# Optimization experiments

Hardware: AMD Instinct MI355X
Metric: run time of the kernel (lower is better)

The kernel has to match this reference:

```python
import jax, jax.numpy as jnp
import numpy as np

BLOCK = 64
# NF4 codebook (normal-float 4-bit values, as in QLoRA/torchao)
NF4_TABLE = jnp.array([
    -1.0, -0.6961928009986877, -0.5250730514526367, -0.39491748809814453,
    -0.28444138169288635, -0.18477343022823334, -0.09105003625154495, 0.0,
    0.07958029955625534, 0.16093020141124725, 0.24611230194568634,
    0.33791524171829224, 0.44070982933044434, 0.5626170039176941,
    0.7229568362236023, 1.0], dtype=jnp.float32)

D_MODEL, HIDDEN = 4096, 11008
BATCH, SEQ = 2, 2048


def setup_inputs() -> dict:
    key = jax.random.key(0)
    ks = jax.random.split(key, 7)
    x = jax.random.normal(ks[0], (BATCH, SEQ, D_MODEL), dtype=jnp.float32)
    w1_q = jax.random.randint(ks[1], (HIDDEN, D_MODEL), 0, 16, dtype=jnp.int32)
    w2_q = jax.random.randint(ks[2], (HIDDEN, D_MODEL), 0, 16, dtype=jnp.int32)
    w3_q = jax.random.randint(ks[3], (D_MODEL, HIDDEN), 0, 16, dtype=jnp.int32)
    # per-block absmax scales (positive, typical weight magnitude ~0.02)
    w1_scale = jax.random.uniform(ks[4], (HIDDEN, D_MODEL // BLOCK), dtype=jnp.float32) * 0.04
    w2_scale = jax.random.uniform(ks[5], (HIDDEN, D_MODEL // BLOCK), dtype=jnp.float32) * 0.04
    w3_scale = jax.random.uniform(ks[6], (D_MODEL, HIDDEN // BLOCK), dtype=jnp.float32) * 0.04
    return {"x": x, "w1_q": w1_q, "w1_scale": w1_scale,
            "w2_q": w2_q, "w2_scale": w2_scale,
            "w3_q": w3_q, "w3_scale": w3_scale}


def dequant_nf4(q, scale):
    # q: [O, I] int codes in [0,16); scale: [O, I//BLOCK]
    O, I = q.shape
    vals = NF4_TABLE[q]                               # lookup -> [O, I]
    vals = vals.reshape(O, I // BLOCK, BLOCK) * scale[:, :, None]
    return vals.reshape(O, I)


def reference(x, w1_q, w1_scale, w2_q, w2_scale, w3_q, w3_scale):
    w1 = dequant_nf4(w1_q, w1_scale)                  # [H, D]
    w2 = dequant_nf4(w2_q, w2_scale)                  # [H, D]
    w3 = dequant_nf4(w3_q, w3_scale)                  # [D, H]
    h = jax.nn.silu(jnp.einsum('bsd,hd->bsh', x, w1)) * jnp.einsum('bsd,hd->bsh', x, w2)
    return jnp.einsum('bsh,dh->bsd', h, w3)
```

## Files before the change

### kernel.cpp

```cpp
#include <hip/hip_runtime.h>
#include <hip/hip_bf16.h>

typedef unsigned short u16;
typedef __bf16  bf16x8 __attribute__((ext_vector_type(8)));
typedef float   f32x4  __attribute__((ext_vector_type(4)));

__device__ __constant__ float NF4C[16] = {
    -1.0f, -0.6961928009986877f, -0.5250730514526367f, -0.39491748809814453f,
    -0.28444138169288635f, -0.18477343022823334f, -0.09105003625154495f, 0.0f,
    0.07958029955625534f, 0.16093020141124725f, 0.24611230194568634f,
    0.33791524171829224f, 0.44070982933044434f, 0.5626170039176941f,
    0.7229568362236023f, 1.0f };

__device__ __forceinline__ u16 f2bf(float f) {
    union { float f; unsigned u; } v; v.f = f;
    unsigned r = v.u + 0x7FFFu + ((v.u >> 16) & 1u);
    return (u16)(r >> 16);
}
__device__ __forceinline__ float bf2f(u16 b) {
    union { unsigned u; float f; } v; v.u = ((unsigned)b) << 16;
    return v.f;
}

__device__ __forceinline__ void gl2lds16(const void* g, void* l) {
    __builtin_amdgcn_global_load_lds(
        (__attribute__((address_space(1))) void*)g,
        (__attribute__((address_space(3))) void*)l,
        16, 0, 0);
}

#define WAITVM(N) asm volatile("s_waitcnt vmcnt(" #N ")" ::: "memory")

__global__ __launch_bounds__(256) void cast_f32_bf16(
    const float* __restrict__ in, u16* __restrict__ out, int n8) {
    int i = blockIdx.x * 256 + threadIdx.x;
    if (i >= n8) return;
    const float4* p = (const float4*)in + (size_t)i * 2;
    float4 a = p[0], b = p[1];
    union { u16 u[8]; uint4 v; } r;
    r.u[0] = f2bf(a.x); r.u[1] = f2bf(a.y); r.u[2] = f2bf(a.z); r.u[3] = f2bf(a.w);
    r.u[4] = f2bf(b.x); r.u[5] = f2bf(b.y); r.u[6] = f2bf(b.z); r.u[7] = f2bf(b.w);
    ((uint4*)out)[i] = r.v;
}

__global__ __launch_bounds__(256) void dequant_nf4(
    const int* __restrict__ q, const float* __restrict__ s,
    u16* __restrict__ w, int I, int spr) {
    __shared__ float tab[16];
    if (threadIdx.x < 16) tab[threadIdx.x] = NF4C[threadIdx.x];
    __syncthreads();
    int col = (blockIdx.x * 256 + threadIdx.x) * 8;
    if (col >= I) return;
    int row = blockIdx.y;
    size_t base = (size_t)row * I + col;
    int4 c0 = *(const int4*)(q + base);
    int4 c1 = *(const int4*)(q + base + 4);
    float sc = s[(size_t)row * spr + (col >> 6)];
    union { u16 u[8]; uint4 v; } r;
    r.u[0] = f2bf(tab[c0.x & 15] * sc);
    r.u[1] = f2bf(tab[c0.y & 15] * sc);
    r.u[2] = f2bf(tab[c0.z & 15] * sc);
    r.u[3] = f2bf(tab[c0.w & 15] * sc);
    r.u[4] = f2bf(tab[c1.x & 15] * sc);
    r.u[5] = f2bf(tab[c1.y & 15] * sc);
    r.u[6] = f2bf(tab[c1.z & 15] * sc);
    r.u[7] = f2bf(tab[c1.w & 15] * sc);
    *(uint4*)(w + base) = r.v;
}

template<int EPI>
__global__ __launch_bounds__(512, 2) void gemm_bt(
    const u16* __restrict__ A, const u16* __restrict__ B,
    void* Cout, const u16* gate, int K, int ldc) {
    __shared__ u16 lA[4 * 8192];
    __shared__ u16 lB[4 * 8192];

    const int tid  = threadIdx.x;
    const int lane = tid & 63;
    const int wv   = tid >> 6;

    const int NT = gridDim.x, MT = gridDim.y;
    int id  = blockIdx.y * NT + blockIdx.x;
    int nid = (id & 7) * ((NT * MT) >> 3) + (id >> 3);
    const int bx = nid / MT;
    const int by = nid - bx * MT;

    const int sr = lane >> 2;
    const int sq = (lane & 3) ^ ((sr >> 1) & 3);
    const u16* gA = A + (size_t)(by * 256 + wv * 16 + sr) * K + (sq << 3);
    const u16* gB = B + (size_t)(bx * 256 + wv * 16 + sr) * K + (sq << 3);
    const size_t half = (size_t)128 * K;
    const int stoff = wv * 512 + lane * 8;

    const int r16    = lane & 15;
    const int pq     = lane >> 4;
    const int slot16 = (r16 << 2) + (pq ^ ((r16 >> 1) & 3));
    const int aFrag  = ((wv & 1) << 3) * 512 + slot16 * 8;
    const int bFrag  = ((wv >> 1) << 2) * 512 + slot16 * 8;

#define STAGE(T) do {                                                   \
        const u16* a_ = gA + (size_t)(T) * 32;                          \
        const u16* b_ = gB + (size_t)(T) * 32;                          \
        u16* la_ = lA + (((T) & 3) << 13) + stoff;                      \
        u16* lb_ = lB + (((T) & 3) << 13) + stoff;                      \
        gl2lds16(a_, la_);                                              \
        gl2lds16(a_ + half, la_ + 8 * 512);                             \
        gl2lds16(b_, lb_);                                              \
        gl2lds16(b_ + half, lb_ + 8 * 512);                             \
    } while (0)

#define COMPUTE(T) do {                                                 \
        const u16* sa_ = lA + (((T) & 3) << 13) + aFrag;                \
        const u16* sb_ = lB + (((T) & 3) << 13) + bFrag;                \
        bf16x8 af[8], bfr[4];                                           \
        _Pragma("unroll")                                               \
        for (int i_ = 0; i_ < 8; ++i_)                                  \
            af[i_] = *(const bf16x8*)(sa_ + i_ * 512);                  \
        _Pragma("unroll")                                               \
        for (int j_ = 0; j_ < 4; ++j_)                                  \
            bfr[j_] = *(const bf16x8*)(sb_ + j_ * 512);                 \
        __builtin_amdgcn_s_setprio(1);                                  \
        _Pragma("unroll")                                               \
        for (int i_ = 0; i_ < 8; ++i_)                                  \
            _Pragma("unroll")                                           \
            for (int j_ = 0; j_ < 4; ++j_)                              \
                acc[i_][j_] = __builtin_amdgcn_mfma_f32_16x16x32_bf16(  \
                    af[i_], bfr[j_], acc[i_][j_], 0, 0, 0);             \
        __builtin_amdgcn_s_setprio(0);                                  \
    } while (0)

#define TILE_BAR() do {                                                 \
        __builtin_amdgcn_s_barrier();                                   \
        __builtin_amdgcn_sched_barrier(0);                              \
    } while (0)

    f32x4 acc[8][4] = {};
    const int KT = K >> 5;

    STAGE(0); STAGE(1); STAGE(2);

    int t = 0;
    for (; t < KT - 3; ++t) {
        WAITVM(8);
        TILE_BAR();
        STAGE(t + 3);
        COMPUTE(t);
    }
    WAITVM(8); TILE_BAR(); COMPUTE(t); ++t;
    WAITVM(4); TILE_BAR(); COMPUTE(t); ++t;
    WAITVM(0); TILE_BAR(); COMPUTE(t);

    const int en   = lane & 15;
    const int er   = (lane >> 4) << 2;
    const int row0 = by * 256 + ((wv & 1) << 7);
    const int col0 = bx * 256 + ((wv >> 1) << 6);
    #pragma unroll
    for (int i = 0; i < 8; ++i) {
        int rowb = row0 + i * 16 + er;
        #pragma unroll
        for (int j = 0; j < 4; ++j) {
            int col = col0 + j * 16 + en;
            #pragma unroll
            for (int r = 0; r < 4; ++r) {
                size_t idx = (size_t)(rowb + r) * ldc + col;
                float v = acc[i][j][r];
                if (EPI == 0) {
                    ((u16*)Cout)[idx] = f2bf(v);
                } else if (EPI == 1) {
                    float g = bf2f(gate[idx]);
                    float sg = g / (1.0f + __expf(-g));
                    ((u16*)Cout)[idx] = f2bf(sg * v);
                } else {
                    ((float*)Cout)[idx] = v;
                }
            }
        }
    }
#undef STAGE
#undef COMPUTE
#undef TILE_BAR
}

extern "C" void kernel_launch(void* const* d_in, const int* in_sizes, int n_in,
                              void* d_out, int out_size, void* d_ws, size_t ws_size,
                              hipStream_t stream) {
    const float* x   = (const float*)d_in[0];
    const int*   w1q = (const int*)d_in[1];
    const float* w1s = (const float*)d_in[2];
    const int*   w2q = (const int*)d_in[3];
    const float* w2s = (const float*)d_in[4];
    const int*   w3q = (const int*)d_in[5];
    const float* w3s = (const float*)d_in[6];
    float* out = (float*)d_out;

    const int M = 4096, D = 4096, H = 11008;

    u16* xb = (u16*)d_ws;
    u16* wb = xb + (size_t)M * D;
    u16* hb = wb + (size_t)H * D;

    cast_f32_bf16<<<(M * D / 8 + 255) / 256, 256, 0, stream>>>(x, xb, M * D / 8);

    dim3 dqg1((D / 8 + 255) / 256, H);
    dequant_nf4<<<dqg1, 256, 0, stream>>>(w1q, w1s, wb, D, D / 64);
    gemm_bt<0><<<dim3(H / 256, M / 256), 512, 0, stream>>>(xb, wb, hb, nullptr, D, H);

    dequant_nf4<<<dqg1, 256, 0, stream>>>(w2q, w2s, wb, D, D / 64);
    gemm_bt<1><<<dim3(H / 256, M / 256), 512, 0, stream>>>(xb, wb, hb, hb, D, H);

    dim3 dqg3((H / 8 + 255) / 256, D);
    dequant_nf4<<<dqg3, 256, 0, stream>>>(w3q, w3s, wb, H, H / 64);
    gemm_bt<2><<<dim3(D / 256, M / 256), 512, 0, stream>>>(hb, wb, out, nullptr, H, D);
}
```

Measured before the change: 2.079 ms.

## Restructure GEMM mainloop into 4-phase ping-pong with K=64 double-buffered tiles

Replaces the 4-stage K=32 pipeline with a double-buffered K=64 tile scheme. Each iteration is split into four quadrant phases, and each phase interleaves LDS fragment reads, partial global->LDS prefetches for upcoming tiles, and a barrier-fenced MFMA burst. The goal is finer-grained overlap of memory traffic with MFMA work and fewer per-K-step loop overheads. In exchange it adds many more barriers per tile, and the loads clamped at the tail redundantly reload the last tile.

```diff
diff --git a/kernel.cpp b/kernel.cpp
--- a/kernel.cpp
+++ b/kernel.cpp
@@ -72,8 +72,8 @@
 __global__ __launch_bounds__(512, 2) void gemm_bt(
     const u16* __restrict__ A, const u16* __restrict__ B,
     void* Cout, const u16* gate, int K, int ldc) {
-    __shared__ u16 lA[4 * 8192];
-    __shared__ u16 lB[4 * 8192];
+    __shared__ u16 lA[2 * 16384];
+    __shared__ u16 lB[2 * 16384];
 
     const int tid  = threadIdx.x;
     const int lane = tid & 63;
@@ -87,68 +87,113 @@
 
     const int sr = lane >> 2;
     const int sq = (lane & 3) ^ ((sr >> 1) & 3);
-    const u16* gA = A + (size_t)(by * 256 + wv * 16 + sr) * K + (sq << 3);
-    const u16* gB = B + (size_t)(bx * 256 + wv * 16 + sr) * K + (sq << 3);
-    const size_t half = (size_t)128 * K;
-    const int stoff = wv * 512 + lane * 8;
+
+    const int gA0 = ((wv & 4) << 1) + (wv & 3);
+    const int gA1 = gA0 + 4;
+    const int gB0 = ((wv >> 1) << 2) + (wv & 1);
+    const int gB1 = gB0 + 2;
+
+    const u16* pA0 = A + (size_t)(by * 256 + gA0 * 16 + sr) * K + (sq << 3);
+    const u16* pA1 = A + (size_t)(by * 256 + gA1 * 16 + sr) * K + (sq << 3);
+    const u16* pB0 = B + (size_t)(bx * 256 + gB0 * 16 + sr) * K + (sq << 3);
+    const u16* pB1 = B + (size_t)(bx * 256 + gB1 * 16 + sr) * K + (sq << 3);
+
+    const int sA0 = gA0 * 512 + lane * 8;
+    const int sA1 = gA1 * 512 + lane * 8;
+    const int sB0 = gB0 * 512 + lane * 8;
+    const int sB1 = gB1 * 512 + lane * 8;
 
     const int r16    = lane & 15;
     const int pq     = lane >> 4;
     const int slot16 = (r16 << 2) + (pq ^ ((r16 >> 1) & 3));
-    const int aFrag  = ((wv & 1) << 3) * 512 + slot16 * 8;
-    const int bFrag  = ((wv >> 1) << 2) * 512 + slot16 * 8;
-
-#define STAGE(T) do {                                                   \
-        const u16* a_ = gA + (size_t)(T) * 32;                          \
-        const u16* b_ = gB + (size_t)(T) * 32;                          \
-        u16* la_ = lA + (((T) & 3) << 13) + stoff;                      \
-        u16* lb_ = lB + (((T) & 3) << 13) + stoff;                      \
-        gl2lds16(a_, la_);                                              \
-        gl2lds16(a_ + half, la_ + 8 * 512);                             \
-        gl2lds16(b_, lb_);                                              \
-        gl2lds16(b_ + half, lb_ + 8 * 512);                             \
-    } while (0)
-
-#define COMPUTE(T) do {                                                 \
-        const u16* sa_ = lA + (((T) & 3) << 13) + aFrag;                \
-        const u16* sb_ = lB + (((T) & 3) << 13) + bFrag;                \
-        bf16x8 af[8], bfr[4];                                           \
-        _Pragma("unroll")                                               \
-        for (int i_ = 0; i_ < 8; ++i_)                                  \
-            af[i_] = *(const bf16x8*)(sa_ + i_ * 512);                  \
-        _Pragma("unroll")                                               \
-        for (int j_ = 0; j_ < 4; ++j_)                                  \
-            bfr[j_] = *(const bf16x8*)(sb_ + j_ * 512);                 \
-        __builtin_amdgcn_s_setprio(1);                                  \
-        _Pragma("unroll")                                               \
-        for (int i_ = 0; i_ < 8; ++i_)                                  \
-            _Pragma("unroll")                                           \
-            for (int j_ = 0; j_ < 4; ++j_)                              \
-                acc[i_][j_] = __builtin_amdgcn_mfma_f32_16x16x32_bf16(  \
-                    af[i_], bfr[j_], acc[i_][j_], 0, 0, 0);             \
-        __builtin_amdgcn_s_setprio(0);                                  \
-    } while (0)
-
-#define TILE_BAR() do {                                                 \
-        __builtin_amdgcn_s_barrier();                                   \
-        __builtin_amdgcn_sched_barrier(0);                              \
-    } while (0)
+    const int aBase  = ((wv & 1) << 12) + slot16 * 8;
+    const int bBase  = ((wv >> 1) << 11) + slot16 * 8;
+
+#define STG_A0(TT, D) do { const u16* g_ = pA0 + (size_t)(TT) * 64;       \
+        u16* l_ = lA + ((D) << 14) + sA0;                                 \
+        gl2lds16(g_, l_); gl2lds16(g_ + 32, l_ + 8192); } while (0)
+#define STG_A1(TT, D) do { const u16* g_ = pA1 + (size_t)(TT) * 64;       \
+        u16* l_ = lA + ((D) << 14) + sA1;                                 \
+        gl2lds16(g_, l_); gl2lds16(g_ + 32, l_ + 8192); } while (0)
+#define STG_B0(TT, D) do { const u16* g_ = pB0 + (size_t)(TT) * 64;       \
+        u16* l_ = lB + ((D) << 14) + sB0;                                 \
+        gl2lds16(g_, l_); gl2lds16(g_ + 32, l_ + 8192); } while (0)
+#define STG_B1(TT, D) do { const u16* g_ = pB1 + (size_t)(TT) * 64;       \
+        u16* l_ = lB + ((D) << 14) + sB1;                                 \
+        gl2lds16(g_, l_); gl2lds16(g_ + 32, l_ + 8192); } while (0)
+
+#define DSR_A(C_, QM) do {                                                \
+        const u16* b_ = lA + ((C_) << 14) + aBase + (QM) * 4 * 512;       \
+        _Pragma("unroll")                                                 \
+        for (int mm = 0; mm < 4; ++mm) {                                  \
+            af[mm * 2 + 0] = *(const bf16x8*)(b_ + mm * 512);             \
+            af[mm * 2 + 1] = *(const bf16x8*)(b_ + mm * 512 + 8192);      \
+        } } while (0)
+#define DSR_B(C_, QN) do {                                                \
+        const u16* b_ = lB + ((C_) << 14) + bBase + (QN) * 2 * 512;       \
+        _Pragma("unroll")                                                 \
+        for (int jj = 0; jj < 2; ++jj) {                                  \
+            bf[(QN) * 4 + jj * 2 + 0] = *(const bf16x8*)(b_ + jj * 512);  \
+            bf[(QN) * 4 + jj * 2 + 1] = *(const bf16x8*)(b_ + jj * 512 + 8192); \
+        } } while (0)
+
+#define MFMA_Q(QM, QN) do {                                               \
+        _Pragma("unroll")                                                 \
+        for (int mm = 0; mm < 4; ++mm)                                    \
+        _Pragma("unroll")                                                 \
+        for (int jj = 0; jj < 2; ++jj) {                                  \
+            f32x4 c_ = acc[(QM) * 4 + mm][(QN) * 2 + jj];                 \
+            c_ = __builtin_amdgcn_mfma_f32_16x16x32_bf16(                 \
+                af[mm * 2 + 0], bf[(QN) * 4 + jj * 2 + 0], c_, 0, 0, 0);  \
+            c_ = __builtin_amdgcn_mfma_f32_16x16x32_bf16(                 \
+                af[mm * 2 + 1], bf[(QN) * 4 + jj * 2 + 1], c_, 0, 0, 0);  \
+            acc[(QM) * 4 + mm][(QN) * 2 + jj] = c_;                       \
+        } } while (0)
+
+#define PH_OPEN() do {                                                    \
+        __builtin_amdgcn_sched_barrier(0);                                \
+        __builtin_amdgcn_s_barrier();                                     \
+        asm volatile("s_waitcnt lgkmcnt(0)" ::: "memory");                \
+        __builtin_amdgcn_sched_barrier(0);                                \
+        __builtin_amdgcn_s_setprio(1); } while (0)
+#define PH_CLOSE() do {                                                   \
+        __builtin_amdgcn_s_setprio(0);                                    \
+        __builtin_amdgcn_sched_barrier(0);                                \
+        __builtin_amdgcn_s_barrier();                                     \
+        __builtin_amdgcn_sched_barrier(0); } while (0)
+#define PH_CLOSE_VM() do {                                                \
+        __builtin_amdgcn_s_setprio(0);                                    \
+        __builtin_amdgcn_sched_barrier(0);                                \
+        WAITVM(4);                                                        \
+        __builtin_amdgcn_s_barrier();                                     \
+        __builtin_amdgcn_sched_barrier(0); } while (0)
 
     f32x4 acc[8][4] = {};
-    const int KT = K >> 5;
-
-    STAGE(0); STAGE(1); STAGE(2);
-
-    int t = 0;
-    for (; t < KT - 3; ++t) {
-        WAITVM(8);
-        TILE_BAR();
-        STAGE(t + 3);
-        COMPUTE(t);
+    bf16x8 af[8], bf[8];
+    const int KT = K >> 6;
+
+    STG_A0(0, 0); STG_B0(0, 0); STG_A1(0, 0); STG_B1(0, 0);
+    STG_A0(1, 1); STG_B0(1, 1);
+    WAITVM(4);
+    __builtin_amdgcn_s_barrier();
+    __builtin_amdgcn_sched_barrier(0);
+
+    for (int T = 0; T < KT; ++T) {
+        const int c  = T & 1, o = c ^ 1;
+        const int t1 = (T + 1 < KT) ? T + 1 : KT - 1;
+        const int t2 = (T + 2 < KT) ? T + 2 : KT - 1;
+        DSR_A(c, 0); DSR_B(c, 0);
+        STG_A1(t1, o);
+        PH_OPEN(); MFMA_Q(0, 0); PH_CLOSE();
+        DSR_B(c, 1);
+        STG_B1(t1, o);
+        PH_OPEN(); MFMA_Q(0, 1); PH_CLOSE();
+        DSR_A(c, 1);
+        STG_A0(t2, c);
+        PH_OPEN(); MFMA_Q(1, 0); PH_CLOSE();
+        STG_B0(t2, c);
+        PH_OPEN(); MFMA_Q(1, 1); PH_CLOSE_VM();
     }
-    WAITVM(8); TILE_BAR(); COMPUTE(t); ++t;
-    WAITVM(4); TILE_BAR(); COMPUTE(t); ++t;
-    WAITVM(0); TILE_BAR(); COMPUTE(t);
 
     const int en   = lane & 15;
     const int er   = (lane >> 4) << 2;
@@ -176,9 +221,16 @@
             }
         }
     }
-#undef STAGE
-#undef COMPUTE
-#undef TILE_BAR
+#undef STG_A0
+#undef STG_A1
+#undef STG_B0
+#undef STG_B1
+#undef DSR_A
+#undef DSR_B
+#undef MFMA_Q
+#undef PH_OPEN
+#undef PH_CLOSE
+#undef PH_CLOSE_VM
 }
 
 extern "C" void kernel_launch(void* const* d_in, const int* in_sizes, int n_in,
```

Measured after the change: 1.794 ms. -13.7%, faster.
